# Performance work log

Measured on AMD Instinct MI355X. Metric: run time of the kernel, lower is better.

The kernel has to match this reference:

```python
import jax, jax.numpy as jnp
import numpy as np

B, C, H, W, NH = 8, 512, 32, 32, 8
HD = C // NH
SCALE = HD ** -0.5


def reshape_for_attention(t, num_heads):
    # faithful to torch: view(B,nh,hd,HW) -> permute(0,3,1,2) -> view(B*nh, HW, hd)
    b, c, h, w = t.shape
    t = t.reshape(b, num_heads, c // num_heads, h * w)
    t = jnp.transpose(t, (0, 3, 1, 2))  # [B, HW, nh, hd]
    return t.reshape(b * num_heads, h * w, c // num_heads)


def reshape_from_attention(t, original_shape, num_heads):
    b, c, h, w = original_shape
    t = t.reshape(b, h * w, num_heads, c // num_heads)
    t = jnp.transpose(t, (0, 2, 3, 1))  # [B, nh, hd, HW]
    return t.reshape(b, c, h, w)


def setup_inputs() -> dict:
    key = jax.random.key(0)
    ks = jax.random.split(key, 6)
    s = (2.0 / C) ** 0.5  # kaiming-ish scale for 1x1 convs
    return {
        "x": jax.random.normal(ks[0], (B, C, H, W), dtype=jnp.float32),
        "wq": jax.random.normal(ks[1], (C, C), dtype=jnp.float32) * s,
        "wk": jax.random.normal(ks[2], (C, C), dtype=jnp.float32) * s,
        "wv": jax.random.normal(ks[3], (C, C), dtype=jnp.float32) * s,
        "wo": jax.random.normal(ks[4], (C, C), dtype=jnp.float32) * s,
        "ln_gamma": jnp.ones((C,), dtype=jnp.float32),
        "ln_beta": jnp.zeros((C,), dtype=jnp.float32),
        "gamma": jnp.zeros((1,), dtype=jnp.float32),
    }


def reference(x, wq, wk, wv, wo, ln_gamma, ln_beta, gamma):
    b, c, h, w = x.shape
    residual = x
    # 1x1 convs, no bias == channel GEMMs
    q = jnp.einsum('oc,bchw->bohw', wq, x)
    k = jnp.einsum('oc,bchw->bohw', wk, x)
    v = jnp.einsum('oc,bchw->bohw', wv, x)
    q = reshape_for_attention(q, NH)  # [B*nh, N, hd]
    k = reshape_for_attention(k, NH)
    v = reshape_for_attention(v, NH)
    attn = jnp.einsum('bnd,bmd->bnm', q, k) * SCALE  # [B*nh, N, N]
    attn = jax.nn.softmax(attn, axis=-1)
    attn_out = jnp.einsum('bnm,bmd->bnd', attn, v)
    attn_out = reshape_from_attention(attn_out, (b, c, h, w), NH)
    out = jnp.einsum('oc,bchw->bohw', wo, attn_out)
    # post-LN over channel dim
    out = jnp.transpose(out, (0, 2, 3, 1))  # [B,H,W,C]
    mu = jnp.mean(out, axis=-1, keepdims=True)
    var = jnp.var(out, axis=-1, keepdims=True)
    out = (out - mu) * jax.lax.rsqrt(var + 1e-5) * ln_gamma + ln_beta
    out = jnp.transpose(out, (0, 3, 1, 2))  # [B,C,H,W]
    return gamma * out + residual
```

## Files before the change

### kernel.cpp

```cpp
#include <hip/hip_runtime.h>
#include <hip/hip_bf16.h>


#define B_  8
#define C_  512
#define N_  1024
#define NH_ 8
#define HD_ 64

typedef __bf16 bf16x8 __attribute__((ext_vector_type(8)));
typedef __bf16 bf16x4 __attribute__((ext_vector_type(4)));
typedef float  f32x4  __attribute__((ext_vector_type(4)));

#define MFMA16(a, b, c) __builtin_amdgcn_mfma_f32_16x16x32_bf16((a), (b), (c), 0, 0, 0)

__device__ __forceinline__ void gload16(const void* g, void* l) {
    __builtin_amdgcn_global_load_lds(
        (const __attribute__((address_space(1))) unsigned int*)g,
        (__attribute__((address_space(3))) unsigned int*)l, 16, 0, 0);
}

__global__ __launch_bounds__(256) void k_prep(const float* __restrict__ x,
                                              const float* __restrict__ wq,
                                              const float* __restrict__ wk,
                                              const float* __restrict__ wv,
                                              const float* __restrict__ wo,
                                              __bf16* __restrict__ xt,
                                              __bf16* __restrict__ wcat) {
    __shared__ float tile[64][68];
    int blk = blockIdx.x;
    int tid = threadIdx.x;
    if (blk < 1024) {
        int b   = blk >> 7;
        int rem = blk & 127;
        int ct  = rem >> 4;
        int pt  = rem & 15;
        int c0 = ct * 64, p0 = pt * 64;
        for (int i = 0; i < 4; ++i) {
            int vi = i * 256 + tid;
            int c = vi >> 4, p4 = (vi & 15) * 4;
            f32x4 v = *(const f32x4*)(x + ((size_t)(b * C_ + c0 + c)) * N_ + p0 + p4);
            *(f32x4*)&tile[c][p4] = v;
        }
        __syncthreads();
        for (int i = 0; i < 4; ++i) {
            int vi = i * 256 + tid;
            int p = vi >> 4, c4 = (vi & 15) * 4;
            bf16x4 v;
            for (int j = 0; j < 4; ++j) v[j] = (__bf16)tile[c4 + j][p];
            *(bf16x4*)(xt + ((size_t)(b * N_ + p0 + p)) * C_ + c0 + c4) = v;
        }
    } else {
        int idx = (blk - 1024) * 256 + tid;
        int mat = idx >> 16;
        int off = (idx & 65535) * 4;
        const float* w = (mat == 0) ? wq : (mat == 1) ? wk : (mat == 2) ? wv : wo;
        f32x4 v = *(const f32x4*)(w + off);
        bf16x4 o;
        for (int j = 0; j < 4; ++j) o[j] = (__bf16)v[j];
        *(bf16x4*)(wcat + (size_t)mat * 262144 + off) = o;
    }
}

__global__ __launch_bounds__(256) void k_qkv(const __bf16* __restrict__ xt,
                                             const __bf16* __restrict__ wcat,
                                             __bf16* __restrict__ qa,
                                             __bf16* __restrict__ ka,
                                             __bf16* __restrict__ vt) {
    __shared__ __bf16 As[3][4096];
    __shared__ __bf16 Bs[3][4096];
    int blk  = blockIdx.x;
    int mat  = blk >> 8;
    int rem  = blk & 255;
    int b    = rem >> 5;
    int tile = rem & 31;
    int tid = threadIdx.x, lane = tid & 63, wid = tid >> 6;
    int quad = lane >> 4, l16 = lane & 15;

    const __bf16* w = wcat + (size_t)mat * 262144;
    const __bf16 *A, *Bm;
    int am0, bn0;
    if (mat < 2) {
        int mt = tile >> 2, nt = tile & 3;
        A   = xt + (size_t)b * N_ * C_;  am0 = mt * 128;
        Bm  = w;                         bn0 = nt * 128;
    } else {
        int mt = tile & 3, nt = tile >> 2;
        A   = w;                         am0 = mt * 128;
        Bm  = xt + (size_t)b * N_ * C_;  bn0 = nt * 128;
    }
    int wr = (wid >> 1) * 64, wc = (wid & 1) * 64;

    int lrow = wid * 16 + (lane >> 2);
    int scol = ((lane & 3) * 16) ^ ((lrow & 3) << 4);
    const char* aS0 = (const char*)A  + (size_t)(am0 + lrow) * 1024 + scol;
    const char* aS1 = aS0 + 65536;
    const char* bS0 = (const char*)Bm + (size_t)(bn0 + lrow) * 1024 + scol;
    const char* bS1 = bS0 + 65536;
    int wb = wid * 1024;

    char *aR = (char*)&As[0][0], *aN = (char*)&As[1][0], *aP = (char*)&As[2][0];
    char *bR = (char*)&Bs[0][0], *bN = (char*)&Bs[1][0], *bP = (char*)&Bs[2][0];

    gload16(aS0,      aR + wb);  gload16(aS1,      aR + wb + 4096);
    gload16(bS0,      bR + wb);  gload16(bS1,      bR + wb + 4096);
    gload16(aS0 + 64, aN + wb);  gload16(aS1 + 64, aN + wb + 4096);
    gload16(bS0 + 64, bN + wb);  gload16(bS1 + 64, bN + wb + 4096);
    asm volatile("s_waitcnt vmcnt(4)" ::: "memory");
    __builtin_amdgcn_s_barrier();

    f32x4 acc[4][4] = {};
    const int fo = (quad * 16) ^ ((l16 & 3) << 4);
    for (int t = 0; t < 16; ++t) {
        int kb = ((t + 2) & 15) * 64;
        gload16(aS0 + kb, aP + wb);  gload16(aS1 + kb, aP + wb + 4096);
        gload16(bS0 + kb, bP + wb);  gload16(bS1 + kb, bP + wb + 4096);

        bf16x8 af[4], bfr[4];
        for (int i = 0; i < 4; ++i)
            af[i]  = *(const bf16x8*)(aR + (wr + i * 16 + l16) * 64 + fo);
        for (int i = 0; i < 4; ++i)
            bfr[i] = *(const bf16x8*)(bR + (wc + i * 16 + l16) * 64 + fo);
        for (int mi = 0; mi < 4; ++mi)
            for (int ni = 0; ni < 4; ++ni)
                acc[mi][ni] = MFMA16(af[mi], bfr[ni], acc[mi][ni]);

        asm volatile("s_waitcnt vmcnt(4)" ::: "memory");
        __builtin_amdgcn_s_barrier();
        char* ta = aR; aR = aN; aN = aP; aP = ta;
        char* tb = bR; bR = bN; bN = bP; bP = tb;
    }

    if (mat < 2) {
        __bf16* dst = (mat == 0) ? qa : ka;
        for (int mi = 0; mi < 4; ++mi)
            for (int r = 0; r < 4; ++r) {
                int p = am0 + wr + mi * 16 + quad * 4 + r;
                int g = b * NH_ + (p >> 7);
                int nbase = (p & 127) * 8;
                for (int ni = 0; ni < 4; ++ni) {
                    int o = bn0 + wc + ni * 16 + l16;
                    dst[((size_t)g * N_ + nbase + (o >> 6)) * HD_ + (o & 63)] =
                        (__bf16)acc[mi][ni][r];
                }
            }
    } else {
        for (int mi = 0; mi < 4; ++mi)
            for (int r = 0; r < 4; ++r) {
                int o = am0 + wr + mi * 16 + quad * 4 + r;
                int m = o & 63, i = o >> 6;
                for (int ni = 0; ni < 4; ++ni) {
                    int p = bn0 + wc + ni * 16 + l16;
                    int g = b * NH_ + (p >> 7);
                    vt[((size_t)g * HD_ + m) * N_ + (p & 127) * 8 + i] =
                        (__bf16)acc[mi][ni][r];
                }
            }
    }
}

__global__ __launch_bounds__(512) void k_attn(const __bf16* __restrict__ qa,
                                              const __bf16* __restrict__ ka,
                                              const __bf16* __restrict__ vt,
                                              __bf16* __restrict__ ap) {
    __shared__ __bf16 Kb[3][4096];
    __shared__ __bf16 Vb[3][4096];
    int blk = blockIdx.x;
    int g  = ((blk & 7) << 3) | ((blk >> 3) & 7);
    int qb = blk >> 6;
    int tid = threadIdx.x, lane = tid & 63, wid = tid >> 6;
    int quad = lane >> 4, l16 = lane & 15;
    int q0 = qb * 256 + wid * 32;

    const __bf16* qp = qa + (size_t)g * N_ * HD_;
    const char* kbb = (const char*)(ka + (size_t)g * N_ * HD_);
    const char* vbb = (const char*)(vt + (size_t)g * HD_ * N_);

    bf16x8 qA0 = *(const bf16x8*)(qp + (size_t)(q0 + l16) * HD_ + quad * 8);
    bf16x8 qA1 = *(const bf16x8*)(qp + (size_t)(q0 + l16) * HD_ + 32 + quad * 8);
    bf16x8 qB0 = *(const bf16x8*)(qp + (size_t)(q0 + 16 + l16) * HD_ + quad * 8);
    bf16x8 qB1 = *(const bf16x8*)(qp + (size_t)(q0 + 16 + l16) * HD_ + 32 + quad * 8);

    int lrow = lane >> 3;
    int scol = ((lane & 7) * 16) ^ (lrow << 4);
    const char* kSrc = kbb + (size_t)(wid * 8 + lrow) * 128  + scol;
    const char* vSrc = vbb + (size_t)(wid * 8 + lrow) * 2048 + scol;
    int wb = wid * 1024;

    char *kR = (char*)&Kb[0][0], *kN = (char*)&Kb[1][0], *kP = (char*)&Kb[2][0];
    char *vR = (char*)&Vb[0][0], *vN = (char*)&Vb[1][0], *vP = (char*)&Vb[2][0];

    gload16(kSrc,        kR + wb);
    gload16(vSrc,        vR + wb);
    gload16(kSrc + 8192, kN + wb);
    gload16(vSrc + 128,  vN + wb);
    asm volatile("s_waitcnt vmcnt(2)" ::: "memory");
    __builtin_amdgcn_s_barrier();

    float liA = 0.f, liB = 0.f;
    f32x4 oA[4] = {}, oB[4] = {};
    const float sc = 0.125f * 1.44269504088896340736f;
    const int fsw  = (l16 & 7) << 4;

    for (int t = 0; t < 16; ++t) {
        int jn = ((t + 2) & 15) * 64;
        gload16(kSrc + (size_t)jn * 128, kP + wb);
        gload16(vSrc + jn * 2,           vP + wb);

        bf16x8 kc0[4], kc1[4];
#pragma unroll
        for (int tt = 0; tt < 4; ++tt) {
            int rb = (tt * 16 + l16) * 128;
            kc0[tt] = *(const bf16x8*)(kR + rb + ((quad * 16) ^ fsw));
            kc1[tt] = *(const bf16x8*)(kR + rb + ((64 + quad * 16) ^ fsw));
        }
        f32x4 sA[4] = {}, sB[4] = {};
#pragma unroll
        for (int tt = 0; tt < 4; ++tt) {
            sA[tt] = MFMA16(kc0[tt], qA0, sA[tt]);
            sA[tt] = MFMA16(kc1[tt], qA1, sA[tt]);
            sB[tt] = MFMA16(kc0[tt], qB0, sB[tt]);
            sB[tt] = MFMA16(kc1[tt], qB1, sB[tt]);
        }

        bf16x8 av[2][4];
#pragma unroll
        for (int h = 0; h < 2; ++h)
#pragma unroll
            for (int dd = 0; dd < 4; ++dd) {
                int rb = (dd * 16 + l16) * 128;
                bf16x4 lo = *(const bf16x4*)(vR + rb + ((h * 64 + quad * 8) ^ fsw));
                bf16x4 hi = *(const bf16x4*)(vR + rb + ((h * 64 + 32 + quad * 8) ^ fsw));
                av[h][dd] = __builtin_shufflevector(lo, hi, 0, 1, 2, 3, 4, 5, 6, 7);
            }

        bf16x8 paf[2], pbf[2];
#pragma unroll
        for (int tt = 0; tt < 4; ++tt)
#pragma unroll
            for (int r = 0; r < 4; ++r) {
                float pvA = exp2f(sA[tt][r] * sc);
                float pvB = exp2f(sB[tt][r] * sc);
                liA += pvA; liB += pvB;
                paf[tt >> 1][(tt & 1) * 4 + r] = (__bf16)pvA;
                pbf[tt >> 1][(tt & 1) * 4 + r] = (__bf16)pvB;
            }

#pragma unroll
        for (int h = 0; h < 2; ++h)
#pragma unroll
            for (int dd = 0; dd < 4; ++dd) {
                oA[dd] = MFMA16(av[h][dd], paf[h], oA[dd]);
                oB[dd] = MFMA16(av[h][dd], pbf[h], oB[dd]);
            }

        asm volatile("s_waitcnt vmcnt(2)" ::: "memory");
        __builtin_amdgcn_s_barrier();
        char* tk = kR; kR = kN; kN = kP; kP = tk;
        char* tv = vR; vR = vN; vN = vP; vP = tv;
    }

    liA += __shfl_xor(liA, 16, 64); liA += __shfl_xor(liA, 32, 64);
    liB += __shfl_xor(liB, 16, 64); liB += __shfl_xor(liB, 32, 64);

    int b = g >> 3, hi = g & 7;
    float invA = 1.0f / liA, invB = 1.0f / liB;
    int nA = q0 + l16, nB = q0 + 16 + l16;
    __bf16* dA = ap + ((size_t)(b * N_ + hi * 128 + (nA >> 3))) * C_ + (nA & 7) * 64;
    __bf16* dB = ap + ((size_t)(b * N_ + hi * 128 + (nB >> 3))) * C_ + (nB & 7) * 64;
#pragma unroll
    for (int dd = 0; dd < 4; ++dd) {
        bf16x4 oa, ob;
#pragma unroll
        for (int r = 0; r < 4; ++r) {
            oa[r] = (__bf16)(oA[dd][r] * invA);
            ob[r] = (__bf16)(oB[dd][r] * invB);
        }
        *(bf16x4*)(dA + dd * 16 + quad * 4) = oa;
        *(bf16x4*)(dB + dd * 16 + quad * 4) = ob;
    }
}

__global__ __launch_bounds__(256) void k_oproj(const __bf16* __restrict__ apm,
                                               const __bf16* __restrict__ wob,
                                               __bf16* __restrict__ o0) {
    __shared__ __bf16 As[3][4096];
    __shared__ __bf16 Bs[3][4096];
    int blk = blockIdx.x;
    int b = blk >> 5, tile = blk & 31;
    int mt = tile >> 2, nt = tile & 3;
    int tid = threadIdx.x, lane = tid & 63, wid = tid >> 6;
    int quad = lane >> 4, l16 = lane & 15;
    int am0 = mt * 128, bn0 = nt * 128;
    int wr = (wid >> 1) * 64, wc = (wid & 1) * 64;
    const __bf16* A = apm + (size_t)b * N_ * C_;

    int lrow = wid * 16 + (lane >> 2);
    int scol = ((lane & 3) * 16) ^ ((lrow & 3) << 4);
    const char* aS0 = (const char*)A   + (size_t)(am0 + lrow) * 1024 + scol;
    const char* aS1 = aS0 + 65536;
    const char* bS0 = (const char*)wob + (size_t)(bn0 + lrow) * 1024 + scol;
    const char* bS1 = bS0 + 65536;
    int wb = wid * 1024;

    char *aR = (char*)&As[0][0], *aN = (char*)&As[1][0], *aP = (char*)&As[2][0];
    char *bR = (char*)&Bs[0][0], *bN = (char*)&Bs[1][0], *bP = (char*)&Bs[2][0];

    gload16(aS0,      aR + wb);  gload16(aS1,      aR + wb + 4096);
    gload16(bS0,      bR + wb);  gload16(bS1,      bR + wb + 4096);
    gload16(aS0 + 64, aN + wb);  gload16(aS1 + 64, aN + wb + 4096);
    gload16(bS0 + 64, bN + wb);  gload16(bS1 + 64, bN + wb + 4096);
    asm volatile("s_waitcnt vmcnt(4)" ::: "memory");
    __builtin_amdgcn_s_barrier();

    f32x4 acc[4][4] = {};
    const int fo = (quad * 16) ^ ((l16 & 3) << 4);
    for (int t = 0; t < 16; ++t) {
        int kb = ((t + 2) & 15) * 64;
        gload16(aS0 + kb, aP + wb);  gload16(aS1 + kb, aP + wb + 4096);
        gload16(bS0 + kb, bP + wb);  gload16(bS1 + kb, bP + wb + 4096);

        bf16x8 af[4], bfr[4];
        for (int i = 0; i < 4; ++i)
            af[i]  = *(const bf16x8*)(aR + (wr + i * 16 + l16) * 64 + fo);
        for (int i = 0; i < 4; ++i)
            bfr[i] = *(const bf16x8*)(bR + (wc + i * 16 + l16) * 64 + fo);
        for (int mi = 0; mi < 4; ++mi)
            for (int ni = 0; ni < 4; ++ni)
                acc[mi][ni] = MFMA16(af[mi], bfr[ni], acc[mi][ni]);

        asm volatile("s_waitcnt vmcnt(4)" ::: "memory");
        __builtin_amdgcn_s_barrier();
        char* ta = aR; aR = aN; aN = aP; aP = ta;
        char* tb = bR; bR = bN; bN = bP; bP = tb;
    }
    for (int mi = 0; mi < 4; ++mi)
        for (int r = 0; r < 4; ++r) {
            int p = am0 + wr + mi * 16 + quad * 4 + r;
            __bf16* dst = o0 + ((size_t)(b * N_ + p)) * C_;
            for (int ni = 0; ni < 4; ++ni)
                dst[bn0 + wc + ni * 16 + l16] = (__bf16)acc[mi][ni][r];
        }
}

__global__ __launch_bounds__(256) void k_ln(const __bf16* __restrict__ o0,
                                            const float* __restrict__ x,
                                            const float* __restrict__ lng,
                                            const float* __restrict__ lnb,
                                            const float* __restrict__ gm,
                                            float* __restrict__ out) {
    __shared__ __bf16 tile[32][C_ + 4];
    int blk = blockIdx.x;
    int b = blk >> 5, pt = blk & 31;
    int p0 = pt * 32;
    int tid = threadIdx.x, lane = tid & 63, wid = tid >> 6;
    float g = gm[0];
    float lg[8], lb[8];
    *(f32x4*)&lg[0] = *(const f32x4*)(lng + lane * 8);
    *(f32x4*)&lg[4] = *(const f32x4*)(lng + lane * 8 + 4);
    *(f32x4*)&lb[0] = *(const f32x4*)(lnb + lane * 8);
    *(f32x4*)&lb[4] = *(const f32x4*)(lnb + lane * 8 + 4);

    for (int i = 0; i < 8; ++i) {
        int p = wid * 8 + i;
        bf16x8 v = *(const bf16x8*)(o0 + ((size_t)(b * N_ + p0 + p)) * C_ + lane * 8);
        float f[8], s = 0.f, ss = 0.f;
        for (int j = 0; j < 8; ++j) { f[j] = (float)v[j]; s += f[j]; ss += f[j] * f[j]; }
        for (int d = 1; d < 64; d <<= 1) { s += __shfl_xor(s, d, 64); ss += __shfl_xor(ss, d, 64); }
        float mean = s * (1.f / 512.f);
        float var  = ss * (1.f / 512.f) - mean * mean;
        float rstd = rsqrtf(fmaxf(var, 0.f) + 1e-5f);
        bf16x4 o1, o2;
        for (int j = 0; j < 4; ++j)
            o1[j] = (__bf16)(g * ((f[j] - mean) * rstd * lg[j] + lb[j]));
        for (int j = 0; j < 4; ++j)
            o2[j] = (__bf16)(g * ((f[j + 4] - mean) * rstd * lg[j + 4] + lb[j + 4]));
        __bf16* dst = &tile[p][lane * 8];
        *(bf16x4*)dst = o1;
        *(bf16x4*)(dst + 4) = o2;
    }
    __syncthreads();
    for (int it = 0; it < 16; ++it) {
        int task = it * 256 + tid;
        int c = task >> 3, p4 = (task & 7) * 4;
        f32x4 xr = *(const f32x4*)(x + ((size_t)(b * C_ + c)) * N_ + p0 + p4);
        f32x4 o;
        for (int j = 0; j < 4; ++j)
            o[j] = (float)tile[p4 + j][c] + xr[j];
        *(f32x4*)(out + ((size_t)(b * C_ + c)) * N_ + p0 + p4) = o;
    }
}

__global__ void k_qkv8f(const float* __restrict__ x, const float* __restrict__ wq,
                        const float* __restrict__ wk, const float* __restrict__ wv,
                        float* __restrict__ qa, float* __restrict__ ka,
                        float* __restrict__ va, int g0) {
    int idx = blockIdx.x * 256 + threadIdx.x;
    int m = idx & 63, n = (idx >> 6) & 1023, Gl = (idx >> 16) & 1, mat = idx >> 17;
    int G = g0 + Gl, b = G >> 3, hb = G & 7;
    int p = hb * 128 + (n >> 3), o = (n & 7) * 64 + m;
    const float* w = (mat == 0) ? wq : (mat == 1) ? wk : wv;
    float acc = 0.f;
    for (int c = 0; c < C_; ++c)
        acc += w[(size_t)o * C_ + c] * x[((size_t)b * C_ + c) * N_ + p];
    float* dst = (mat == 0) ? qa : (mat == 1) ? ka : va;
    dst[((size_t)Gl * N_ + n) * HD_ + m] = acc;
}
__global__ void k_attn8f(const float* __restrict__ qa, const float* __restrict__ ka,
                         const float* __restrict__ va, float* __restrict__ ac, int g0) {
    int idx = blockIdx.x * 256 + threadIdx.x;
    int i = idx & 1023, Gl = (idx >> 10) & 1, G = g0 + Gl;
    const float* qrow = qa + ((size_t)Gl * N_ + i) * HD_;
    float q[HD_];
    for (int m = 0; m < HD_; ++m) q[m] = qrow[m];
    const float* kb = ka + (size_t)Gl * N_ * HD_;
    const float* vb = va + (size_t)Gl * N_ * HD_;
    float mx = -1e30f;
    for (int j = 0; j < N_; ++j) {
        float s = 0.f;
        for (int m = 0; m < HD_; ++m) s += q[m] * kb[j * HD_ + m];
        mx = fmaxf(mx, s);
    }
    mx *= 0.125f;
    float l = 0.f, ov[HD_];
    for (int m = 0; m < HD_; ++m) ov[m] = 0.f;
    for (int j = 0; j < N_; ++j) {
        float s = 0.f;
        for (int m = 0; m < HD_; ++m) s += q[m] * kb[j * HD_ + m];
        float pj = __expf(s * 0.125f - mx);
        l += pj;
        for (int m = 0; m < HD_; ++m) ov[m] += pj * vb[j * HD_ + m];
    }
    float inv = 1.0f / l;
    int b = G >> 3, hb = G & 7;
    int p = hb * 128 + (i >> 3), cb = (i & 7) * 64;
    for (int m = 0; m < HD_; ++m)
        ac[((size_t)b * C_ + cb + m) * N_ + p] = ov[m] * inv;
}
__global__ void k_oln8f(float* __restrict__ ac, const float* __restrict__ wo,
                        const float* __restrict__ x, const float* __restrict__ lng,
                        const float* __restrict__ lnb, const float* __restrict__ gm) {
    int tid = threadIdx.x, lane = tid & 63, wid = tid >> 6;
    int bp = blockIdx.x * 4 + wid;
    int b = bp >> 10, p = bp & 1023;
    float oc[8];
    for (int h = 0; h < 8; ++h) oc[h] = 0.f;
    for (int c = 0; c < C_; ++c) {
        float cv = ac[((size_t)b * C_ + c) * N_ + p];
        for (int h = 0; h < 8; ++h)
            oc[h] += wo[(size_t)(h * 64 + lane) * C_ + c] * cv;
    }
    float s = 0.f, ss = 0.f;
    for (int h = 0; h < 8; ++h) { s += oc[h]; ss += oc[h] * oc[h]; }
    for (int d = 1; d < 64; d <<= 1) { s += __shfl_xor(s, d, 64); ss += __shfl_xor(ss, d, 64); }
    float mean = s * (1.f / 512.f);
    float var  = ss * (1.f / 512.f) - mean * mean;
    float rstd = rsqrtf(fmaxf(var, 0.f) + 1e-5f);
    float g = gm[0];
    for (int h = 0; h < 8; ++h) {
        int o = h * 64 + lane;
        float xv = x[((size_t)b * C_ + o) * N_ + p];
        ac[((size_t)b * C_ + o) * N_ + p] =
            g * ((oc[h] - mean) * rstd * lng[o] + lnb[o]) + xv;
    }
}

extern "C" void kernel_launch(void* const* d_in, const int* in_sizes, int n_in,
                              void* d_out, int out_size, void* d_ws, size_t ws_size,
                              hipStream_t stream) {
    const float* x   = (const float*)d_in[0];
    const float* wq  = (const float*)d_in[1];
    const float* wk  = (const float*)d_in[2];
    const float* wv  = (const float*)d_in[3];
    const float* wo  = (const float*)d_in[4];
    const float* lng = (const float*)d_in[5];
    const float* lnb = (const float*)d_in[6];
    const float* gm  = (const float*)d_in[7];
    float* out = (float*)d_out;
    char* wsb = (char*)d_ws;

    if (ws_size >= ((size_t)18 << 20)) {
        __bf16* xt   = (__bf16*)wsb;
        __bf16* wcat = (__bf16*)(wsb + ((size_t)8 << 20));
        __bf16* Qa   = (__bf16*)(wsb + ((size_t)10 << 20));
        __bf16* Ka   = (__bf16*)d_out;
        __bf16* VaT  = (__bf16*)((char*)d_out + ((size_t)8 << 20));
        __bf16* ap   = xt;
        __bf16* o0   = Qa;
        __bf16* wob  = wcat + 3 * 262144;

        k_prep  <<<2048, 256, 0, stream>>>(x, wq, wk, wv, wo, xt, wcat);
        k_qkv   <<<768,  256, 0, stream>>>(xt, wcat, Qa, Ka, VaT);
        k_attn  <<<256,  512, 0, stream>>>(Qa, Ka, VaT, ap);
        k_oproj <<<256,  256, 0, stream>>>(ap, wob, o0);
        k_ln    <<<256,  256, 0, stream>>>(o0, x, lng, lnb, gm, out);
    } else {
        float* qa = (float*)(wsb + 256);
        float* ka = qa + 2 * N_ * HD_;
        float* va = ka + 2 * N_ * HD_;
        for (int g0 = 0; g0 < 64; g0 += 2) {
            k_qkv8f <<<1536, 256, 0, stream>>>(x, wq, wk, wv, qa, ka, va, g0);
            k_attn8f<<<8,    256, 0, stream>>>(qa, ka, va, out, g0);
        }
        k_oln8f<<<2048, 256, 0, stream>>>(out, wo, x, lng, lnb, gm);
    }
}
```

Baseline: 163.7 us.

## Fold softmax scale into Q projection and process two KV tiles per barrier

```diff
diff --git a/kernel.cpp b/kernel.cpp
--- a/kernel.cpp
+++ b/kernel.cpp
@@ -133,6 +133,7 @@
 
     if (mat < 2) {
         __bf16* dst = (mat == 0) ? qa : ka;
+        float scl = (mat == 0) ? 0.18033688011112042f : 1.0f;
         for (int mi = 0; mi < 4; ++mi)
             for (int r = 0; r < 4; ++r) {
                 int p = am0 + wr + mi * 16 + quad * 4 + r;
@@ -141,7 +142,7 @@
                 for (int ni = 0; ni < 4; ++ni) {
                     int o = bn0 + wc + ni * 16 + l16;
                     dst[((size_t)g * N_ + nbase + (o >> 6)) * HD_ + (o & 63)] =
-                        (__bf16)acc[mi][ni][r];
+                        (__bf16)(acc[mi][ni][r] * scl);
                 }
             }
     } else {
@@ -163,8 +164,8 @@
                                               const __bf16* __restrict__ ka,
                                               const __bf16* __restrict__ vt,
                                               __bf16* __restrict__ ap) {
-    __shared__ __bf16 Kb[3][4096];
-    __shared__ __bf16 Vb[3][4096];
+    __shared__ __bf16 Kb[6][4096];
+    __shared__ __bf16 Vb[6][4096];
     int blk = blockIdx.x;
     int g  = ((blk & 7) << 3) | ((blk >> 3) & 7);
     int qb = blk >> 6;
@@ -187,77 +188,131 @@
     const char* vSrc = vbb + (size_t)(wid * 8 + lrow) * 2048 + scol;
     int wb = wid * 1024;
 
-    char *kR = (char*)&Kb[0][0], *kN = (char*)&Kb[1][0], *kP = (char*)&Kb[2][0];
-    char *vR = (char*)&Vb[0][0], *vN = (char*)&Vb[1][0], *vP = (char*)&Vb[2][0];
-
-    gload16(kSrc,        kR + wb);
-    gload16(vSrc,        vR + wb);
-    gload16(kSrc + 8192, kN + wb);
-    gload16(vSrc + 128,  vN + wb);
-    asm volatile("s_waitcnt vmcnt(2)" ::: "memory");
+    char *k0 = (char*)&Kb[0][0], *k1 = (char*)&Kb[1][0], *k2 = (char*)&Kb[2][0];
+    char *k3 = (char*)&Kb[3][0], *k4 = (char*)&Kb[4][0], *k5 = (char*)&Kb[5][0];
+    char *v0 = (char*)&Vb[0][0], *v1 = (char*)&Vb[1][0], *v2 = (char*)&Vb[2][0];
+    char *v3 = (char*)&Vb[3][0], *v4 = (char*)&Vb[4][0], *v5 = (char*)&Vb[5][0];
+
+    gload16(kSrc,             k0 + wb);
+    gload16(vSrc,             v0 + wb);
+    gload16(kSrc + 8192,      k1 + wb);
+    gload16(vSrc + 128,       v1 + wb);
+    gload16(kSrc + 2 * 8192,  k2 + wb);
+    gload16(vSrc + 2 * 128,   v2 + wb);
+    gload16(kSrc + 3 * 8192,  k3 + wb);
+    gload16(vSrc + 3 * 128,   v3 + wb);
+    asm volatile("s_waitcnt vmcnt(4)" ::: "memory");
     __builtin_amdgcn_s_barrier();
 
     float liA = 0.f, liB = 0.f;
     f32x4 oA[4] = {}, oB[4] = {};
-    const float sc = 0.125f * 1.44269504088896340736f;
-    const int fsw  = (l16 & 7) << 4;
-
-    for (int t = 0; t < 16; ++t) {
-        int jn = ((t + 2) & 15) * 64;
-        gload16(kSrc + (size_t)jn * 128, kP + wb);
-        gload16(vSrc + jn * 2,           vP + wb);
-
-        bf16x8 kc0[4], kc1[4];
-#pragma unroll
-        for (int tt = 0; tt < 4; ++tt) {
-            int rb = (tt * 16 + l16) * 128;
-            kc0[tt] = *(const bf16x8*)(kR + rb + ((quad * 16) ^ fsw));
-            kc1[tt] = *(const bf16x8*)(kR + rb + ((64 + quad * 16) ^ fsw));
-        }
-        f32x4 sA[4] = {}, sB[4] = {};
-#pragma unroll
-        for (int tt = 0; tt < 4; ++tt) {
-            sA[tt] = MFMA16(kc0[tt], qA0, sA[tt]);
-            sA[tt] = MFMA16(kc1[tt], qA1, sA[tt]);
-            sB[tt] = MFMA16(kc0[tt], qB0, sB[tt]);
-            sB[tt] = MFMA16(kc1[tt], qB1, sB[tt]);
-        }
-
-        bf16x8 av[2][4];
-#pragma unroll
-        for (int h = 0; h < 2; ++h)
-#pragma unroll
-            for (int dd = 0; dd < 4; ++dd) {
-                int rb = (dd * 16 + l16) * 128;
-                bf16x4 lo = *(const bf16x4*)(vR + rb + ((h * 64 + quad * 8) ^ fsw));
-                bf16x4 hi = *(const bf16x4*)(vR + rb + ((h * 64 + 32 + quad * 8) ^ fsw));
-                av[h][dd] = __builtin_shufflevector(lo, hi, 0, 1, 2, 3, 4, 5, 6, 7);
+    const int fsw = (l16 & 7) << 4;
+
+    for (int i = 0; i < 8; ++i) {
+        int j4 = ((2 * i + 4) & 15) * 64;
+        int j5 = ((2 * i + 5) & 15) * 64;
+        gload16(kSrc + (size_t)j4 * 128, k4 + wb);
+        gload16(vSrc + j4 * 2,           v4 + wb);
+        gload16(kSrc + (size_t)j5 * 128, k5 + wb);
+        gload16(vSrc + j5 * 2,           v5 + wb);
+
+        {
+            bf16x8 kc0[4], kc1[4];
+#pragma unroll
+            for (int tt = 0; tt < 4; ++tt) {
+                int rb = (tt * 16 + l16) * 128;
+                kc0[tt] = *(const bf16x8*)(k0 + rb + ((quad * 16) ^ fsw));
+                kc1[tt] = *(const bf16x8*)(k0 + rb + ((64 + quad * 16) ^ fsw));
             }
-
-        bf16x8 paf[2], pbf[2];
-#pragma unroll
-        for (int tt = 0; tt < 4; ++tt)
-#pragma unroll
-            for (int r = 0; r < 4; ++r) {
-                float pvA = exp2f(sA[tt][r] * sc);
-                float pvB = exp2f(sB[tt][r] * sc);
-                liA += pvA; liB += pvB;
-                paf[tt >> 1][(tt & 1) * 4 + r] = (__bf16)pvA;
-                pbf[tt >> 1][(tt & 1) * 4 + r] = (__bf16)pvB;
+            f32x4 sA[4] = {}, sB[4] = {};
+#pragma unroll
+            for (int tt = 0; tt < 4; ++tt) {
+                sA[tt] = MFMA16(kc0[tt], qA0, sA[tt]);
+                sA[tt] = MFMA16(kc1[tt], qA1, sA[tt]);
+                sB[tt] = MFMA16(kc0[tt], qB0, sB[tt]);
+                sB[tt] = MFMA16(kc1[tt], qB1, sB[tt]);
             }
-
-#pragma unroll
-        for (int h = 0; h < 2; ++h)
-#pragma unroll
-            for (int dd = 0; dd < 4; ++dd) {
-                oA[dd] = MFMA16(av[h][dd], paf[h], oA[dd]);
-                oB[dd] = MFMA16(av[h][dd], pbf[h], oB[dd]);
+            bf16x8 av[2][4];
+#pragma unroll
+            for (int h = 0; h < 2; ++h)
+#pragma unroll
+                for (int dd = 0; dd < 4; ++dd) {
+                    int rb = (dd * 16 + l16) * 128;
+                    bf16x4 lo = *(const bf16x4*)(v0 + rb + ((h * 64 + quad * 8) ^ fsw));
+                    bf16x4 hi = *(const bf16x4*)(v0 + rb + ((h * 64 + 32 + quad * 8) ^ fsw));
+                    av[h][dd] = __builtin_shufflevector(lo, hi, 0, 1, 2, 3, 4, 5, 6, 7);
+                }
+            bf16x8 paf[2], pbf[2];
+#pragma unroll
+            for (int tt = 0; tt < 4; ++tt)
+#pragma unroll
+                for (int r = 0; r < 4; ++r) {
+                    float pvA = exp2f(sA[tt][r]);
+                    float pvB = exp2f(sB[tt][r]);
+                    liA += pvA; liB += pvB;
+                    paf[tt >> 1][(tt & 1) * 4 + r] = (__bf16)pvA;
+                    pbf[tt >> 1][(tt & 1) * 4 + r] = (__bf16)pvB;
+                }
+#pragma unroll
+            for (int h = 0; h < 2; ++h)
+#pragma unroll
+                for (int dd = 0; dd < 4; ++dd) {
+                    oA[dd] = MFMA16(av[h][dd], paf[h], oA[dd]);
+                    oB[dd] = MFMA16(av[h][dd], pbf[h], oB[dd]);
+                }
+        }
+        {
+            bf16x8 kc0[4], kc1[4];
+#pragma unroll
+            for (int tt = 0; tt < 4; ++tt) {
+                int rb = (tt * 16 + l16) * 128;
+                kc0[tt] = *(const bf16x8*)(k1 + rb + ((quad * 16) ^ fsw));
+                kc1[tt] = *(const bf16x8*)(k1 + rb + ((64 + quad * 16) ^ fsw));
             }
-
-        asm volatile("s_waitcnt vmcnt(2)" ::: "memory");
+            f32x4 sA[4] = {}, sB[4] = {};
+#pragma unroll
+            for (int tt = 0; tt < 4; ++tt) {
+                sA[tt] = MFMA16(kc0[tt], qA0, sA[tt]);
+                sA[tt] = MFMA16(kc1[tt], qA1, sA[tt]);
+                sB[tt] = MFMA16(kc0[tt], qB0, sB[tt]);
+                sB[tt] = MFMA16(kc1[tt], qB1, sB[tt]);
+            }
+            bf16x8 av[2][4];
+#pragma unroll
+            for (int h = 0; h < 2; ++h)
+#pragma unroll
+                for (int dd = 0; dd < 4; ++dd) {
+                    int rb = (dd * 16 + l16) * 128;
+                    bf16x4 lo = *(const bf16x4*)(v1 + rb + ((h * 64 + quad * 8) ^ fsw));
+                    bf16x4 hi = *(const bf16x4*)(v1 + rb + ((h * 64 + 32 + quad * 8) ^ fsw));
+                    av[h][dd] = __builtin_shufflevector(lo, hi, 0, 1, 2, 3, 4, 5, 6, 7);
+                }
+            bf16x8 paf[2], pbf[2];
+#pragma unroll
+            for (int tt = 0; tt < 4; ++tt)
+#pragma unroll
+                for (int r = 0; r < 4; ++r) {
+                    float pvA = exp2f(sA[tt][r]);
+                    float pvB = exp2f(sB[tt][r]);
+                    liA += pvA; liB += pvB;
+                    paf[tt >> 1][(tt & 1) * 4 + r] = (__bf16)pvA;
+                    pbf[tt >> 1][(tt & 1) * 4 + r] = (__bf16)pvB;
+                }
+#pragma unroll
+            for (int h = 0; h < 2; ++h)
+#pragma unroll
+                for (int dd = 0; dd < 4; ++dd) {
+                    oA[dd] = MFMA16(av[h][dd], paf[h], oA[dd]);
+                    oB[dd] = MFMA16(av[h][dd], pbf[h], oB[dd]);
+                }
+        }
+
+        asm volatile("s_waitcnt vmcnt(4)" ::: "memory");
         __builtin_amdgcn_s_barrier();
-        char* tk = kR; kR = kN; kN = kP; kP = tk;
-        char* tv = vR; vR = vN; vN = vP; vP = tv;
+        char* tk0 = k0; char* tk1 = k1;
+        k0 = k2; k1 = k3; k2 = k4; k3 = k5; k4 = tk0; k5 = tk1;
+        char* tv0 = v0; char* tv1 = v1;
+        v0 = v2; v1 = v3; v2 = v4; v3 = v5; v4 = tv0; v5 = tv1;
     }
 
     liA += __shfl_xor(liA, 16, 64); liA += __shfl_xor(liA, 32, 64);
```

New measurement: 167.9 us. 2.5% more time.

## Fuse output projection with LayerNorm epilogue and fold softmax scale into Q

Applied to the files above, without the earlier changes.

```diff
diff --git a/kernel.cpp b/kernel.cpp
--- a/kernel.cpp
+++ b/kernel.cpp
@@ -133,6 +133,7 @@
 
     if (mat < 2) {
         __bf16* dst = (mat == 0) ? qa : ka;
+        float scl = (mat == 0) ? 0.18033688011112042f : 1.0f;
         for (int mi = 0; mi < 4; ++mi)
             for (int r = 0; r < 4; ++r) {
                 int p = am0 + wr + mi * 16 + quad * 4 + r;
@@ -141,7 +142,7 @@
                 for (int ni = 0; ni < 4; ++ni) {
                     int o = bn0 + wc + ni * 16 + l16;
                     dst[((size_t)g * N_ + nbase + (o >> 6)) * HD_ + (o & 63)] =
-                        (__bf16)acc[mi][ni][r];
+                        (__bf16)(acc[mi][ni][r] * scl);
                 }
             }
     } else {
@@ -199,8 +200,7 @@
 
     float liA = 0.f, liB = 0.f;
     f32x4 oA[4] = {}, oB[4] = {};
-    const float sc = 0.125f * 1.44269504088896340736f;
-    const int fsw  = (l16 & 7) << 4;
+    const int fsw = (l16 & 7) << 4;
 
     for (int t = 0; t < 16; ++t) {
         int jn = ((t + 2) & 15) * 64;
@@ -239,8 +239,8 @@
         for (int tt = 0; tt < 4; ++tt)
 #pragma unroll
             for (int r = 0; r < 4; ++r) {
-                float pvA = exp2f(sA[tt][r] * sc);
-                float pvB = exp2f(sB[tt][r] * sc);
+                float pvA = exp2f(sA[tt][r]);
+                float pvB = exp2f(sB[tt][r]);
                 liA += pvA; liB += pvB;
                 paf[tt >> 1][(tt & 1) * 4 + r] = (__bf16)pvA;
                 pbf[tt >> 1][(tt & 1) * 4 + r] = (__bf16)pvB;
@@ -281,114 +281,136 @@
     }
 }
 
-__global__ __launch_bounds__(256) void k_oproj(const __bf16* __restrict__ apm,
-                                               const __bf16* __restrict__ wob,
-                                               __bf16* __restrict__ o0) {
-    __shared__ __bf16 As[3][4096];
-    __shared__ __bf16 Bs[3][4096];
+__global__ __launch_bounds__(512) void k_oln(const __bf16* __restrict__ apm,
+                                             const __bf16* __restrict__ wob,
+                                             const float* __restrict__ x,
+                                             const float* __restrict__ lng,
+                                             const float* __restrict__ lnb,
+                                             const float* __restrict__ gm,
+                                             float* __restrict__ out) {
+    __shared__ __bf16 As[3][1024];
+    __shared__ __bf16 Bs[3][16384];
+    __shared__ float  psum[8][32][2];
     int blk = blockIdx.x;
-    int b = blk >> 5, tile = blk & 31;
-    int mt = tile >> 2, nt = tile & 3;
+    int b = blk >> 5, pt = blk & 31;
     int tid = threadIdx.x, lane = tid & 63, wid = tid >> 6;
     int quad = lane >> 4, l16 = lane & 15;
-    int am0 = mt * 128, bn0 = nt * 128;
-    int wr = (wid >> 1) * 64, wc = (wid & 1) * 64;
-    const __bf16* A = apm + (size_t)b * N_ * C_;
-
-    int lrow = wid * 16 + (lane >> 2);
-    int scol = ((lane & 3) * 16) ^ ((lrow & 3) << 4);
-    const char* aS0 = (const char*)A   + (size_t)(am0 + lrow) * 1024 + scol;
-    const char* aS1 = aS0 + 65536;
-    const char* bS0 = (const char*)wob + (size_t)(bn0 + lrow) * 1024 + scol;
-    const char* bS1 = bS0 + 65536;
-    int wb = wid * 1024;
+    float gv = gm[0];
+
+    int arow = wid * 4 + (lane >> 2);
+    int brow = wid * 16 + (lane >> 2);
+    int scol = ((lane & 3) * 16) ^ (((lane >> 2) & 3) << 4);
+    const char* aSrc = (const char*)apm + (size_t)(b * N_ + pt * 32 + arow) * 1024 + scol;
+    const char* bSrc = (const char*)wob + (size_t)brow * 1024 + scol;
 
     char *aR = (char*)&As[0][0], *aN = (char*)&As[1][0], *aP = (char*)&As[2][0];
     char *bR = (char*)&Bs[0][0], *bN = (char*)&Bs[1][0], *bP = (char*)&Bs[2][0];
-
-    gload16(aS0,      aR + wb);  gload16(aS1,      aR + wb + 4096);
-    gload16(bS0,      bR + wb);  gload16(bS1,      bR + wb + 4096);
-    gload16(aS0 + 64, aN + wb);  gload16(aS1 + 64, aN + wb + 4096);
-    gload16(bS0 + 64, bN + wb);  gload16(bS1 + 64, bN + wb + 4096);
-    asm volatile("s_waitcnt vmcnt(4)" ::: "memory");
+    int awb = wid * 256;
+    int bwb = wid * 1024;
+
+    if (lane < 16) gload16(aSrc, aR + awb);
+#pragma unroll
+    for (int j = 0; j < 4; ++j)
+        gload16(bSrc + (size_t)j * 131072, bR + j * 8192 + bwb);
+    if (lane < 16) gload16(aSrc + 64, aN + awb);
+#pragma unroll
+    for (int j = 0; j < 4; ++j)
+        gload16(bSrc + (size_t)j * 131072 + 64, bN + j * 8192 + bwb);
+    asm volatile("s_waitcnt vmcnt(5)" ::: "memory");
     __builtin_amdgcn_s_barrier();
 
-    f32x4 acc[4][4] = {};
+    f32x4 acc[2][4] = {};
     const int fo = (quad * 16) ^ ((l16 & 3) << 4);
     for (int t = 0; t < 16; ++t) {
         int kb = ((t + 2) & 15) * 64;
-        gload16(aS0 + kb, aP + wb);  gload16(aS1 + kb, aP + wb + 4096);
-        gload16(bS0 + kb, bP + wb);  gload16(bS1 + kb, bP + wb + 4096);
-
-        bf16x8 af[4], bfr[4];
+        if (lane < 16) gload16(aSrc + kb, aP + awb);
+#pragma unroll
+        for (int j = 0; j < 4; ++j)
+            gload16(bSrc + (size_t)j * 131072 + kb, bP + j * 8192 + bwb);
+
+        bf16x8 af[2], bfr[4];
+#pragma unroll
+        for (int i = 0; i < 2; ++i)
+            af[i]  = *(const bf16x8*)(aR + (i * 16 + l16) * 64 + fo);
+#pragma unroll
         for (int i = 0; i < 4; ++i)
-            af[i]  = *(const bf16x8*)(aR + (wr + i * 16 + l16) * 64 + fo);
-        for (int i = 0; i < 4; ++i)
-            bfr[i] = *(const bf16x8*)(bR + (wc + i * 16 + l16) * 64 + fo);
-        for (int mi = 0; mi < 4; ++mi)
+            bfr[i] = *(const bf16x8*)(bR + (wid * 64 + i * 16 + l16) * 64 + fo);
+#pragma unroll
+        for (int mi = 0; mi < 2; ++mi)
+#pragma unroll
             for (int ni = 0; ni < 4; ++ni)
                 acc[mi][ni] = MFMA16(af[mi], bfr[ni], acc[mi][ni]);
 
-        asm volatile("s_waitcnt vmcnt(4)" ::: "memory");
+        asm volatile("s_waitcnt vmcnt(5)" ::: "memory");
         __builtin_amdgcn_s_barrier();
         char* ta = aR; aR = aN; aN = aP; aP = ta;
         char* tb = bR; bR = bN; bN = bP; bP = tb;
     }
-    for (int mi = 0; mi < 4; ++mi)
+
+    float sm[2][4], sq[2][4];
+#pragma unroll
+    for (int mi = 0; mi < 2; ++mi)
+#pragma unroll
         for (int r = 0; r < 4; ++r) {
-            int p = am0 + wr + mi * 16 + quad * 4 + r;
-            __bf16* dst = o0 + ((size_t)(b * N_ + p)) * C_;
-            for (int ni = 0; ni < 4; ++ni)
-                dst[bn0 + wc + ni * 16 + l16] = (__bf16)acc[mi][ni][r];
-        }
-}
-
-__global__ __launch_bounds__(256) void k_ln(const __bf16* __restrict__ o0,
-                                            const float* __restrict__ x,
-                                            const float* __restrict__ lng,
-                                            const float* __restrict__ lnb,
-                                            const float* __restrict__ gm,
-                                            float* __restrict__ out) {
-    __shared__ __bf16 tile[32][C_ + 4];
-    int blk = blockIdx.x;
-    int b = blk >> 5, pt = blk & 31;
-    int p0 = pt * 32;
-    int tid = threadIdx.x, lane = tid & 63, wid = tid >> 6;
-    float g = gm[0];
-    float lg[8], lb[8];
-    *(f32x4*)&lg[0] = *(const f32x4*)(lng + lane * 8);
-    *(f32x4*)&lg[4] = *(const f32x4*)(lng + lane * 8 + 4);
-    *(f32x4*)&lb[0] = *(const f32x4*)(lnb + lane * 8);
-    *(f32x4*)&lb[4] = *(const f32x4*)(lnb + lane * 8 + 4);
-
-    for (int i = 0; i < 8; ++i) {
-        int p = wid * 8 + i;
-        bf16x8 v = *(const bf16x8*)(o0 + ((size_t)(b * N_ + p0 + p)) * C_ + lane * 8);
-        float f[8], s = 0.f, ss = 0.f;
-        for (int j = 0; j < 8; ++j) { f[j] = (float)v[j]; s += f[j]; ss += f[j] * f[j]; }
-        for (int d = 1; d < 64; d <<= 1) { s += __shfl_xor(s, d, 64); ss += __shfl_xor(ss, d, 64); }
-        float mean = s * (1.f / 512.f);
-        float var  = ss * (1.f / 512.f) - mean * mean;
-        float rstd = rsqrtf(fmaxf(var, 0.f) + 1e-5f);
-        bf16x4 o1, o2;
-        for (int j = 0; j < 4; ++j)
-            o1[j] = (__bf16)(g * ((f[j] - mean) * rstd * lg[j] + lb[j]));
-        for (int j = 0; j < 4; ++j)
-            o2[j] = (__bf16)(g * ((f[j + 4] - mean) * rstd * lg[j + 4] + lb[j + 4]));
-        __bf16* dst = &tile[p][lane * 8];
-        *(bf16x4*)dst = o1;
-        *(bf16x4*)(dst + 4) = o2;
+            float s = 0.f, q = 0.f;
+#pragma unroll
+            for (int ni = 0; ni < 4; ++ni) {
+                float v = acc[mi][ni][r];
+                s += v; q += v * v;
+            }
+            s += __shfl_xor(s, 1, 64);  q += __shfl_xor(q, 1, 64);
+            s += __shfl_xor(s, 2, 64);  q += __shfl_xor(q, 2, 64);
+            s += __shfl_xor(s, 4, 64);  q += __shfl_xor(q, 4, 64);
+            s += __shfl_xor(s, 8, 64);  q += __shfl_xor(q, 8, 64);
+            sm[mi][r] = s; sq[mi][r] = q;
+        }
+    if (l16 == 0) {
+#pragma unroll
+        for (int mi = 0; mi < 2; ++mi)
+#pragma unroll
+            for (int r = 0; r < 4; ++r) {
+                int p = mi * 16 + quad * 4 + r;
+                psum[wid][p][0] = sm[mi][r];
+                psum[wid][p][1] = sq[mi][r];
+            }
     }
     __syncthreads();
-    for (int it = 0; it < 16; ++it) {
-        int task = it * 256 + tid;
-        int c = task >> 3, p4 = (task & 7) * 4;
-        f32x4 xr = *(const f32x4*)(x + ((size_t)(b * C_ + c)) * N_ + p0 + p4);
-        f32x4 o;
-        for (int j = 0; j < 4; ++j)
-            o[j] = (float)tile[p4 + j][c] + xr[j];
-        *(f32x4*)(out + ((size_t)(b * C_ + c)) * N_ + p0 + p4) = o;
-    }
+
+    float mean[2][4], rstd[2][4];
+#pragma unroll
+    for (int mi = 0; mi < 2; ++mi)
+#pragma unroll
+        for (int r = 0; r < 4; ++r) {
+            int p = mi * 16 + quad * 4 + r;
+            float S = 0.f, Q = 0.f;
+#pragma unroll
+            for (int w = 0; w < 8; ++w) { S += psum[w][p][0]; Q += psum[w][p][1]; }
+            float mn  = S * (1.f / 512.f);
+            float var = Q * (1.f / 512.f) - mn * mn;
+            mean[mi][r] = mn;
+            rstd[mi][r] = rsqrtf(fmaxf(var, 0.f) + 1e-5f);
+        }
+
+    float lgv[4], lbv[4];
+#pragma unroll
+    for (int ni = 0; ni < 4; ++ni) {
+        int c = wid * 64 + ni * 16 + l16;
+        lgv[ni] = lng[c]; lbv[ni] = lnb[c];
+    }
+#pragma unroll
+    for (int mi = 0; mi < 2; ++mi)
+#pragma unroll
+        for (int ni = 0; ni < 4; ++ni) {
+            int c = wid * 64 + ni * 16 + l16;
+            size_t base = ((size_t)(b * C_ + c)) * N_ + pt * 32 + mi * 16 + quad * 4;
+            f32x4 xr = *(const f32x4*)(x + base);
+            f32x4 o;
+#pragma unroll
+            for (int r = 0; r < 4; ++r)
+                o[r] = gv * ((acc[mi][ni][r] - mean[mi][r]) * rstd[mi][r] * lgv[ni]
+                             + lbv[ni]) + xr[r];
+            *(f32x4*)(out + base) = o;
+        }
 }
 
 __global__ void k_qkv8f(const float* __restrict__ x, const float* __restrict__ wq,
@@ -486,14 +508,12 @@
         __bf16* Ka   = (__bf16*)d_out;
         __bf16* VaT  = (__bf16*)((char*)d_out + ((size_t)8 << 20));
         __bf16* ap   = xt;
-        __bf16* o0   = Qa;
         __bf16* wob  = wcat + 3 * 262144;
 
-        k_prep  <<<2048, 256, 0, stream>>>(x, wq, wk, wv, wo, xt, wcat);
-        k_qkv   <<<768,  256, 0, stream>>>(xt, wcat, Qa, Ka, VaT);
-        k_attn  <<<256,  512, 0, stream>>>(Qa, Ka, VaT, ap);
-        k_oproj <<<256,  256, 0, stream>>>(ap, wob, o0);
-        k_ln    <<<256,  256, 0, stream>>>(o0, x, lng, lnb, gm, out);
+        k_prep <<<2048, 256, 0, stream>>>(x, wq, wk, wv, wo, xt, wcat);
+        k_qkv  <<<768,  256, 0, stream>>>(xt, wcat, Qa, Ka, VaT);
+        k_attn <<<256,  512, 0, stream>>>(Qa, Ka, VaT, ap);
+        k_oln  <<<256,  512, 0, stream>>>(ap, wob, x, lng, lnb, gm, out);
     } else {
         float* qa = (float*)(wsb + 256);
         float* ka = qa + 2 * N_ * HD_;
```

After: 162.5 us (median of 2 runs). About the same (-0.7%).
